# Performance work log

Measured on AMD Instinct MI355X. Metric: run time of the kernel, lower is better.

The kernel has to match this reference:

```python
import jax, jax.numpy as jnp
import numpy as np

W_IN = 128
I_DIM = 64
O_DIM = 64
B = 256
W = 64


def setup_inputs() -> dict:
    key = jax.random.key(0)
    ks = jax.random.split(key, 12)
    std = 0.01
    inp = {
        "input": jax.random.normal(ks[0], (B, W, I_DIM), jnp.float32),
        "w_embeddings": jax.random.normal(ks[1], (B, W, W_IN), jnp.float32),
        "logj": jax.random.normal(ks[2], (B, W, I_DIM), jnp.float32),
        # w_net: Linear(W_IN -> 2*W_IN), Tanh, Linear(2*W_IN -> I*O)
        "w_w1": jax.random.normal(ks[3], (2 * W_IN, W_IN), jnp.float32) * std,
        "w_b1": jnp.zeros((2 * W_IN,), jnp.float32),
        "w_w2": jax.random.normal(ks[4], (I_DIM * O_DIM, 2 * W_IN), jnp.float32) * std,
        "w_b2": jnp.zeros((I_DIM * O_DIM,), jnp.float32),
        # b_net: Linear(W_IN -> 2*W_IN), Tanh, Linear(2*W_IN -> O)
        "b_w1": jax.random.normal(ks[5], (2 * W_IN, W_IN), jnp.float32) * std,
        "b_b1": jnp.zeros((2 * W_IN,), jnp.float32),
        "b_w2": jax.random.normal(ks[6], (O_DIM, 2 * W_IN), jnp.float32) * std,
        "b_b2": jnp.zeros((O_DIM,), jnp.float32),
    }
    return inp


def reference(input, w_embeddings, logj, w_w1, w_b1, w_w2, w_b2, b_w1, b_b1, b_w2, b_b2):
    # Hypernetworks: two small MLPs over w_embeddings [B, W, W_IN]
    h_w = jnp.tanh(jnp.einsum('bwe,he->bwh', w_embeddings, w_w1) + w_b1)
    w1 = (jnp.einsum('bwh,oh->bwo', h_w, w_w2) + w_b2).reshape(B, W, I_DIM, O_DIM)

    h_b = jnp.tanh(jnp.einsum('bwe,he->bwh', w_embeddings, b_w1) + b_b1)
    b1 = jnp.einsum('bwh,oh->bwo', h_b, b_w2) + b_b2  # [B, W, O]

    # exp-weighted contraction: output[b,w,o] = sum_i input[b,w,i] * exp(w1[b,w,i,o]) + b1
    output = jnp.einsum('bwi,bwio->bwo', input, jnp.exp(w1)) + b1

    # log-Jacobian accumulation: logsumexp over input dim
    logj_out = jax.nn.logsumexp(w1 + logj[..., None], axis=-2)  # [B, W, O]
    return (output, logj_out)
```

## Files before the change

kernel.cpp:

```cpp
#include <hip/hip_runtime.h>
#include <math.h>


typedef __attribute__((ext_vector_type(8))) short s16x8;
typedef __attribute__((ext_vector_type(4))) float f32x4;

__device__ inline unsigned short f2bf(float f) {
  unsigned int u = __float_as_uint(f);
  u += 0x7fffu + ((u >> 16) & 1u);
  return (unsigned short)(u >> 16);
}
__device__ inline float bf2f(unsigned short u) { return __uint_as_float(((unsigned int)u) << 16); }
__device__ inline s16x8 cvt8(float4 a, float4 b) {
  s16x8 v;
  v[0] = (short)f2bf(a.x); v[1] = (short)f2bf(a.y); v[2] = (short)f2bf(a.z); v[3] = (short)f2bf(a.w);
  v[4] = (short)f2bf(b.x); v[5] = (short)f2bf(b.y); v[6] = (short)f2bf(b.z); v[7] = (short)f2bf(b.w);
  return v;
}
__device__ inline float fast_tanh(float x) {
  float t = __expf(2.0f * x);
  return __fdividef(t - 1.0f, t + 1.0f);
}
__device__ inline void stage16(const unsigned short* gsrc, char* ldst) {
  __builtin_amdgcn_global_load_lds(
      (const __attribute__((address_space(1))) unsigned int*)gsrc,
      (__attribute__((address_space(3))) unsigned int*)ldst, 16, 0, 0);
}

__global__ __launch_bounds__(256) void k_pre(
    const float* __restrict__ w_w2, const float* __restrict__ emb,
    const float* __restrict__ w_w1, const float* __restrict__ w_b1,
    const float* __restrict__ b_w1, const float* __restrict__ b_b1,
    const float* __restrict__ b_w2, const float* __restrict__ b_b2,
    unsigned short* __restrict__ W2F, unsigned short* __restrict__ Hw,
    float* __restrict__ b1out) {
  __shared__ __align__(16) char lsm[67584];
  const int t = threadIdx.x, l = t & 63, lo = t & 15, hi = (t >> 4) & 3, w = t >> 6;
  const int bid = blockIdx.x;

  if (bid < 64) {
    const int i = bid;
    float* ld = (float*)lsm;
    const float* src = w_w2 + (size_t)i * 16384;
    #pragma unroll
    for (int v = 0; v < 16; ++v) {
      int flat = t * 64 + v * 4;
      int row = flat >> 8, col = flat & 255;
      *(float4*)(ld + row * 264 + col) = *(const float4*)(src + flat);
    }
    __syncthreads();
    #pragma unroll
    for (int ks = 0; ks < 8; ++ks) {
      const float* p = ld + (w * 16 + lo) * 264 + ks * 32 + hi * 8;
      s16x8 vfr = cvt8(*(const float4*)p, *(const float4*)(p + 4));
      *(s16x8*)(W2F + ((size_t)(i * 4 + w) * 8 + ks) * 512 + (size_t)l * 8) = vfr;
    }
    return;
  }

  const int hb_id = bid - 64, net = hb_id & 1, mb = hb_id >> 1;
  const int mw0 = mb * 128 + w * 32;
  const float* W1 = net ? b_w1 : w_w1;
  const float* B1 = net ? b_b1 : w_b1;
  s16x8 ae[2][4];
  #pragma unroll
  for (int mt = 0; mt < 2; ++mt)
    #pragma unroll
    for (int ks = 0; ks < 4; ++ks) {
      const float* p = emb + (size_t)(mw0 + mt * 16 + lo) * 128 + ks * 32 + hi * 8;
      ae[mt][ks] = cvt8(*(const float4*)p, *(const float4*)(p + 4));
    }
  unsigned short* hb = (unsigned short*)lsm + (size_t)w * 32 * 264;
  #pragma unroll
  for (int nt = 0; nt < 16; ++nt) {
    f32x4 acc[2] = {{0,0,0,0},{0,0,0,0}};
    #pragma unroll
    for (int ks = 0; ks < 4; ++ks) {
      const float* bp = W1 + (size_t)(nt * 16 + lo) * 128 + ks * 32 + hi * 8;
      s16x8 bf = cvt8(*(const float4*)bp, *(const float4*)(bp + 4));
      acc[0] = __builtin_amdgcn_mfma_f32_16x16x32_bf16(ae[0][ks], bf, acc[0], 0, 0, 0);
      acc[1] = __builtin_amdgcn_mfma_f32_16x16x32_bf16(ae[1][ks], bf, acc[1], 0, 0, 0);
    }
    float bv = B1[nt * 16 + lo];
    #pragma unroll
    for (int mt = 0; mt < 2; ++mt)
      #pragma unroll
      for (int r = 0; r < 4; ++r) {
        float h = fast_tanh(acc[mt][r] + bv);
        if (net) hb[(mt * 16 + hi * 4 + r) * 264 + nt * 16 + lo] = f2bf(h);
        else Hw[(size_t)(mw0 + mt * 16 + hi * 4 + r) * 256 + nt * 16 + lo] = f2bf(h);
      }
  }
  if (net) {
    #pragma unroll
    for (int ot = 0; ot < 4; ++ot) {
      f32x4 acc[2] = {{0,0,0,0},{0,0,0,0}};
      #pragma unroll
      for (int ks = 0; ks < 8; ++ks) {
        const float* bp = b_w2 + (size_t)(ot * 16 + lo) * 256 + ks * 32 + hi * 8;
        s16x8 bf = cvt8(*(const float4*)bp, *(const float4*)(bp + 4));
        s16x8 a0 = *(const s16x8*)(hb + (0 * 16 + lo) * 264 + ks * 32 + hi * 8);
        s16x8 a1 = *(const s16x8*)(hb + (1 * 16 + lo) * 264 + ks * 32 + hi * 8);
        acc[0] = __builtin_amdgcn_mfma_f32_16x16x32_bf16(a0, bf, acc[0], 0, 0, 0);
        acc[1] = __builtin_amdgcn_mfma_f32_16x16x32_bf16(a1, bf, acc[1], 0, 0, 0);
      }
      float bb = b_b2[ot * 16 + lo];
      #pragma unroll
      for (int mt = 0; mt < 2; ++mt)
        #pragma unroll
        for (int r = 0; r < 4; ++r)
          b1out[(size_t)(mw0 + mt * 16 + hi * 4 + r) * 64 + ot * 16 + lo] = acc[mt][r] + bb;
    }
  }
}

__global__ __launch_bounds__(256, 2) void k_fused(
    const float* __restrict__ input, const float* __restrict__ logj,
    const float* __restrict__ w_b2,
    const unsigned short* __restrict__ W2F, const unsigned short* __restrict__ Hw,
    float* __restrict__ Poa, float* __restrict__ Pse) {
  __shared__ __align__(16) char smem[81920];
  float* xin_l = (float*)(smem + 65536);
  unsigned short* elj_l = (unsigned short*)(smem + 73728);
  unsigned short* ewb_l = (unsigned short*)(smem + 77824);

  const int t = threadIdx.x, l = t & 63, lo = t & 15, hi = (t >> 4) & 3;
  const int w = t >> 6, wu = __builtin_amdgcn_readfirstlane(w);
  const int bid = blockIdx.x;
  const int mb = bid >> 1, iq = bid & 1;
  const int m0 = mb * 64, i0 = iq * 32;

  {
    int mm = t & 63, ib = (t >> 6) * 8;
    const float* ip = input + (size_t)(m0 + mm) * 64 + i0 + ib;
    const float* lp = logj + (size_t)(m0 + mm) * 64 + i0 + ib;
    float4 v0 = *(const float4*)ip, v1 = *(const float4*)(ip + 4);
    float4 g0 = *(const float4*)lp, g1 = *(const float4*)(lp + 4);
    float vi[8] = {v0.x, v0.y, v0.z, v0.w, v1.x, v1.y, v1.z, v1.w};
    float gj[8] = {g0.x, g0.y, g0.z, g0.w, g1.x, g1.y, g1.z, g1.w};
    #pragma unroll
    for (int j = 0; j < 8; ++j) {
      xin_l[(ib + j) * 64 + mm] = vi[j];
      elj_l[(ib + j) * 64 + mm] = f2bf(__expf(gj[j]));
    }
    int il = t >> 3, ob = (t & 7) * 8;
    const float* wp = w_b2 + (size_t)(i0 + il) * 64 + ob;
    float4 e0 = *(const float4*)wp, e1 = *(const float4*)(wp + 4);
    float ev[8] = {e0.x, e0.y, e0.z, e0.w, e1.x, e1.y, e1.z, e1.w};
    #pragma unroll
    for (int j = 0; j < 8; ++j) ewb_l[il * 64 + ob + j] = f2bf(__expf(ev[j]));
  }

  s16x8 bh[4][8];
  #pragma unroll
  for (int nt = 0; nt < 4; ++nt)
    #pragma unroll
    for (int ks = 0; ks < 8; ++ks)
      bh[nt][ks] = *(const s16x8*)(Hw + (size_t)(m0 + nt * 16 + lo) * 256 + ks * 32 + hi * 8);

  __syncthreads();

  char* Ab = smem + wu * 16384;
  #pragma unroll
  for (int p = 0; p < 2; ++p)
    #pragma unroll
    for (int ks = 0; ks < 8; ++ks)
      stage16(W2F + ((size_t)(i0 + p) * 4 + wu) * 4096 + ks * 512 + (size_t)l * 8,
              Ab + p * 8192 + ks * 1024);

  f32x4 outa[4] = {{0,0,0,0},{0,0,0,0},{0,0,0,0},{0,0,0,0}};
  f32x4 sea[4] = {{0,0,0,0},{0,0,0,0},{0,0,0,0},{0,0,0,0}};

  for (int il = 0; il < 32; ++il) {
    if (il < 31) asm volatile("s_waitcnt vmcnt(8)" ::: "memory");
    else         asm volatile("s_waitcnt vmcnt(0)" ::: "memory");
    __builtin_amdgcn_sched_barrier(0);
    const char* ab = Ab + (il & 1) * 8192;

    float xin[4], el[4], ew[4];
    #pragma unroll
    for (int nt = 0; nt < 4; ++nt) {
      xin[nt] = xin_l[il * 64 + nt * 16 + lo];
      el[nt] = bf2f(elj_l[il * 64 + nt * 16 + lo]);
    }
    {
      ushort4 uv = *(const ushort4*)(ewb_l + il * 64 + wu * 16 + hi * 4);
      ew[0] = bf2f(uv.x); ew[1] = bf2f(uv.y); ew[2] = bf2f(uv.z); ew[3] = bf2f(uv.w);
    }
    f32x4 acc[4] = {{0,0,0,0},{0,0,0,0},{0,0,0,0},{0,0,0,0}};
    #pragma unroll
    for (int ks = 0; ks < 8; ++ks) {
      s16x8 a = *(const s16x8*)(ab + ks * 1024 + l * 16);
      acc[0] = __builtin_amdgcn_mfma_f32_16x16x32_bf16(a, bh[0][ks], acc[0], 0, 0, 0);
      acc[1] = __builtin_amdgcn_mfma_f32_16x16x32_bf16(a, bh[1][ks], acc[1], 0, 0, 0);
      acc[2] = __builtin_amdgcn_mfma_f32_16x16x32_bf16(a, bh[2][ks], acc[2], 0, 0, 0);
      acc[3] = __builtin_amdgcn_mfma_f32_16x16x32_bf16(a, bh[3][ks], acc[3], 0, 0, 0);
    }
    asm volatile("s_waitcnt lgkmcnt(0)" ::: "memory");
    __builtin_amdgcn_sched_barrier(0);
    if (il < 30) {
      size_t gb = ((size_t)(i0 + il + 2) * 4 + wu) * 4096;
      #pragma unroll
      for (int ks = 0; ks < 8; ++ks)
        stage16(W2F + gb + ks * 512 + (size_t)l * 8, Ab + (il & 1) * 8192 + ks * 1024);
    }
    #pragma unroll
    for (int nt = 0; nt < 4; ++nt)
      #pragma unroll
      for (int r = 0; r < 4; ++r) {
        float e1 = __expf(acc[nt][r]) * ew[r];
        outa[nt][r] = fmaf(xin[nt], e1, outa[nt][r]);
        sea[nt][r] = fmaf(el[nt], e1, sea[nt][r]);
      }
  }

  const int o0 = wu * 16 + hi * 4;
  #pragma unroll
  for (int nt = 0; nt < 4; ++nt) {
    size_t base = (size_t)(m0 + nt * 16 + lo) * 64 + o0;
    *(f32x4*)(Poa + (size_t)iq * 1048576 + base) = outa[nt];
    *(f32x4*)(Pse + (size_t)iq * 1048576 + base) = sea[nt];
  }
}

__global__ __launch_bounds__(256) void k_final(
    const float* __restrict__ b1, const float* __restrict__ Poa,
    const float* __restrict__ Pse, float* __restrict__ out) {
  int idx = (blockIdx.x * 256 + threadIdx.x) * 4;
  float4 bb = *(const float4*)(b1 + idx);
  float4 a0 = *(const float4*)(Poa + idx);
  float4 a1 = *(const float4*)(Poa + 1048576 + idx);
  float4 s0 = *(const float4*)(Pse + idx);
  float4 s1 = *(const float4*)(Pse + 1048576 + idx);
  float4 o1, o2;
  o1.x = bb.x + a0.x + a1.x; o1.y = bb.y + a0.y + a1.y;
  o1.z = bb.z + a0.z + a1.z; o1.w = bb.w + a0.w + a1.w;
  o2.x = __logf(s0.x + s1.x); o2.y = __logf(s0.y + s1.y);
  o2.z = __logf(s0.z + s1.z); o2.w = __logf(s0.w + s1.w);
  *(float4*)(out + idx) = o1;
  *(float4*)(out + 1048576 + idx) = o2;
}

extern "C" void kernel_launch(void* const* d_in, const int* in_sizes, int n_in,
                              void* d_out, int out_size, void* d_ws, size_t ws_size,
                              hipStream_t stream) {
  const float* input = (const float*)d_in[0];
  const float* w_emb = (const float*)d_in[1];
  const float* logj  = (const float*)d_in[2];
  const float* w_w1  = (const float*)d_in[3];
  const float* w_b1  = (const float*)d_in[4];
  const float* w_w2  = (const float*)d_in[5];
  const float* w_b2  = (const float*)d_in[6];
  const float* b_w1  = (const float*)d_in[7];
  const float* b_b1  = (const float*)d_in[8];
  const float* b_w2  = (const float*)d_in[9];
  const float* b_b2  = (const float*)d_in[10];
  float* out = (float*)d_out;

  char* wsb = (char*)d_ws;
  unsigned short* W2F = (unsigned short*)(wsb);
  unsigned short* Hw  = (unsigned short*)(wsb + 2097152);
  float*          b1  = (float*)(wsb + 10485760);
  float*          Poa = (float*)(wsb + 14680064);
  float*          Pse = (float*)(wsb + 23068672);

  hipLaunchKernelGGL(k_pre, dim3(320), dim3(256), 0, stream,
                     w_w2, w_emb, w_w1, w_b1, b_w1, b_b1, b_w2, b_b2, W2F, Hw, b1);
  hipLaunchKernelGGL(k_fused, dim3(512), dim3(256), 0, stream,
                     input, logj, w_b2, W2F, Hw, Poa, Pse);
  hipLaunchKernelGGL(k_final, dim3(1024), dim3(256), 0, stream, b1, Poa, Pse, out);
}
```

Before: 160.4 us.

## Split W2 staging into half-chunks, shrink pre-kernel row tiles, cache W1 in LDS

In the fused kernel, each 8-chunk W2F stage is split into two halves with separate vmcnt waits, so MFMAs on the first half can start while the second half is still loading. In the pre-kernel, each wave now handles 16 rows instead of 32 and the grid doubles to 576 blocks, raising parallelism. W1 is converted to bf16 once per block into LDS rather than reloaded from global per wave. The W2 transpose load is made coalesced, and the b_net hidden state stays in registers before a single LDS write. The cost is more waitcnt bookkeeping that must track the issue order of outstanding loads.

```diff
diff --git a/kernel.cpp b/kernel.cpp
--- a/kernel.cpp
+++ b/kernel.cpp
@@ -4,6 +4,8 @@
 
 typedef __attribute__((ext_vector_type(8))) short s16x8;
 typedef __attribute__((ext_vector_type(4))) float f32x4;
+
+#define WAITV(N) asm volatile("s_waitcnt vmcnt(" #N ")" ::: "memory")
 
 __device__ inline unsigned short f2bf(float f) {
   unsigned int u = __float_as_uint(f);
@@ -36,6 +38,7 @@
     float* __restrict__ b1out) {
   __shared__ __align__(16) char lsm[67584];
   const int t = threadIdx.x, l = t & 63, lo = t & 15, hi = (t >> 4) & 3, w = t >> 6;
+  const int wu = __builtin_amdgcn_readfirstlane(w);
   const int bid = blockIdx.x;
 
   if (bid < 64) {
@@ -44,7 +47,7 @@
     const float* src = w_w2 + (size_t)i * 16384;
     #pragma unroll
     for (int v = 0; v < 16; ++v) {
-      int flat = t * 64 + v * 4;
+      int flat = v * 1024 + t * 4;
       int row = flat >> 8, col = flat & 255;
       *(float4*)(ld + row * 264 + col) = *(const float4*)(src + flat);
     }
@@ -59,57 +62,68 @@
   }
 
   const int hb_id = bid - 64, net = hb_id & 1, mb = hb_id >> 1;
-  const int mw0 = mb * 128 + w * 32;
+  const int mw0 = mb * 64 + w * 16;
   const float* W1 = net ? b_w1 : w_w1;
   const float* B1 = net ? b_b1 : w_b1;
-  s16x8 ae[2][4];
-  #pragma unroll
-  for (int mt = 0; mt < 2; ++mt)
+
+  #pragma unroll
+  for (int j = 0; j < 16; ++j) {
+    int c = wu * 16 + j, nt = c >> 2, ks = c & 3;
+    const float* bp = W1 + (size_t)(nt * 16 + lo) * 128 + ks * 32 + hi * 8;
+    s16x8 f = cvt8(*(const float4*)bp, *(const float4*)(bp + 4));
+    *(s16x8*)(lsm + c * 1024 + l * 16) = f;
+  }
+  s16x8 ae[4];
+  #pragma unroll
+  for (int ks = 0; ks < 4; ++ks) {
+    const float* p = emb + (size_t)(mw0 + lo) * 128 + ks * 32 + hi * 8;
+    ae[ks] = cvt8(*(const float4*)p, *(const float4*)(p + 4));
+  }
+  __syncthreads();
+
+  unsigned short hreg[16][4];
+  #pragma unroll
+  for (int nt = 0; nt < 16; ++nt) {
+    f32x4 acc = {0.f, 0.f, 0.f, 0.f};
     #pragma unroll
     for (int ks = 0; ks < 4; ++ks) {
-      const float* p = emb + (size_t)(mw0 + mt * 16 + lo) * 128 + ks * 32 + hi * 8;
-      ae[mt][ks] = cvt8(*(const float4*)p, *(const float4*)(p + 4));
-    }
-  unsigned short* hb = (unsigned short*)lsm + (size_t)w * 32 * 264;
-  #pragma unroll
-  for (int nt = 0; nt < 16; ++nt) {
-    f32x4 acc[2] = {{0,0,0,0},{0,0,0,0}};
-    #pragma unroll
-    for (int ks = 0; ks < 4; ++ks) {
-      const float* bp = W1 + (size_t)(nt * 16 + lo) * 128 + ks * 32 + hi * 8;
-      s16x8 bf = cvt8(*(const float4*)bp, *(const float4*)(bp + 4));
-      acc[0] = __builtin_amdgcn_mfma_f32_16x16x32_bf16(ae[0][ks], bf, acc[0], 0, 0, 0);
-      acc[1] = __builtin_amdgcn_mfma_f32_16x16x32_bf16(ae[1][ks], bf, acc[1], 0, 0, 0);
+      s16x8 b = *(const s16x8*)(lsm + (nt * 4 + ks) * 1024 + l * 16);
+      acc = __builtin_amdgcn_mfma_f32_16x16x32_bf16(ae[ks], b, acc, 0, 0, 0);
     }
     float bv = B1[nt * 16 + lo];
     #pragma unroll
-    for (int mt = 0; mt < 2; ++mt)
-      #pragma unroll
-      for (int r = 0; r < 4; ++r) {
-        float h = fast_tanh(acc[mt][r] + bv);
-        if (net) hb[(mt * 16 + hi * 4 + r) * 264 + nt * 16 + lo] = f2bf(h);
-        else Hw[(size_t)(mw0 + mt * 16 + hi * 4 + r) * 256 + nt * 16 + lo] = f2bf(h);
-      }
+    for (int r = 0; r < 4; ++r) {
+      float h = fast_tanh(acc[r] + bv);
+      if (net) hreg[nt][r] = f2bf(h);
+      else Hw[(size_t)(mw0 + hi * 4 + r) * 256 + nt * 16 + lo] = f2bf(h);
+    }
   }
   if (net) {
+    __syncthreads();
+    unsigned short* hb = (unsigned short*)(lsm) + (size_t)wu * 4224;
+    #pragma unroll
+    for (int nt = 0; nt < 16; ++nt)
+      #pragma unroll
+      for (int r = 0; r < 4; ++r)
+        hb[(hi * 4 + r) * 264 + nt * 16 + lo] = hreg[nt][r];
+    s16x8 ab[8];
+    __builtin_amdgcn_s_waitcnt(0);
+    #pragma unroll
+    for (int ks = 0; ks < 8; ++ks)
+      ab[ks] = *(const s16x8*)(hb + lo * 264 + ks * 32 + hi * 8);
     #pragma unroll
     for (int ot = 0; ot < 4; ++ot) {
-      f32x4 acc[2] = {{0,0,0,0},{0,0,0,0}};
+      f32x4 acc2 = {0.f, 0.f, 0.f, 0.f};
       #pragma unroll
       for (int ks = 0; ks < 8; ++ks) {
         const float* bp = b_w2 + (size_t)(ot * 16 + lo) * 256 + ks * 32 + hi * 8;
         s16x8 bf = cvt8(*(const float4*)bp, *(const float4*)(bp + 4));
-        s16x8 a0 = *(const s16x8*)(hb + (0 * 16 + lo) * 264 + ks * 32 + hi * 8);
-        s16x8 a1 = *(const s16x8*)(hb + (1 * 16 + lo) * 264 + ks * 32 + hi * 8);
-        acc[0] = __builtin_amdgcn_mfma_f32_16x16x32_bf16(a0, bf, acc[0], 0, 0, 0);
-        acc[1] = __builtin_amdgcn_mfma_f32_16x16x32_bf16(a1, bf, acc[1], 0, 0, 0);
+        acc2 = __builtin_amdgcn_mfma_f32_16x16x32_bf16(ab[ks], bf, acc2, 0, 0, 0);
       }
       float bb = b_b2[ot * 16 + lo];
       #pragma unroll
-      for (int mt = 0; mt < 2; ++mt)
-        #pragma unroll
-        for (int r = 0; r < 4; ++r)
-          b1out[(size_t)(mw0 + mt * 16 + hi * 4 + r) * 64 + ot * 16 + lo] = acc[mt][r] + bb;
+      for (int r = 0; r < 4; ++r)
+        b1out[(size_t)(mw0 + hi * 4 + r) * 64 + ot * 16 + lo] = acc2[r] + bb;
     }
   }
 }
@@ -159,24 +173,19 @@
       bh[nt][ks] = *(const s16x8*)(Hw + (size_t)(m0 + nt * 16 + lo) * 256 + ks * 32 + hi * 8);
 
   __syncthreads();
+  asm volatile("s_waitcnt vmcnt(0)" ::: "memory");
+  __builtin_amdgcn_sched_barrier(0);
 
   char* Ab = smem + wu * 16384;
   #pragma unroll
-  for (int p = 0; p < 2; ++p)
-    #pragma unroll
-    for (int ks = 0; ks < 8; ++ks)
-      stage16(W2F + ((size_t)(i0 + p) * 4 + wu) * 4096 + ks * 512 + (size_t)l * 8,
-              Ab + p * 8192 + ks * 1024);
+  for (int g = 0; g < 16; ++g)
+    stage16(W2F + ((size_t)(i0 + (g >> 3)) * 4 + wu) * 4096 + (size_t)(g & 7) * 512 + (size_t)l * 8,
+            Ab + g * 1024);
 
   f32x4 outa[4] = {{0,0,0,0},{0,0,0,0},{0,0,0,0},{0,0,0,0}};
   f32x4 sea[4] = {{0,0,0,0},{0,0,0,0},{0,0,0,0},{0,0,0,0}};
 
   for (int il = 0; il < 32; ++il) {
-    if (il < 31) asm volatile("s_waitcnt vmcnt(8)" ::: "memory");
-    else         asm volatile("s_waitcnt vmcnt(0)" ::: "memory");
-    __builtin_amdgcn_sched_barrier(0);
-    const char* ab = Ab + (il & 1) * 8192;
-
     float xin[4], el[4], ew[4];
     #pragma unroll
     for (int nt = 0; nt < 4; ++nt) {
@@ -188,8 +197,12 @@
       ew[0] = bf2f(uv.x); ew[1] = bf2f(uv.y); ew[2] = bf2f(uv.z); ew[3] = bf2f(uv.w);
     }
     f32x4 acc[4] = {{0,0,0,0},{0,0,0,0},{0,0,0,0},{0,0,0,0}};
-    #pragma unroll
-    for (int ks = 0; ks < 8; ++ks) {
+    char* ab = Ab + (il & 1) * 8192;
+
+    if (il < 31) { WAITV(12); } else { WAITV(4); }
+    __builtin_amdgcn_sched_barrier(0);
+    #pragma unroll
+    for (int ks = 0; ks < 4; ++ks) {
       s16x8 a = *(const s16x8*)(ab + ks * 1024 + l * 16);
       acc[0] = __builtin_amdgcn_mfma_f32_16x16x32_bf16(a, bh[0][ks], acc[0], 0, 0, 0);
       acc[1] = __builtin_amdgcn_mfma_f32_16x16x32_bf16(a, bh[1][ks], acc[1], 0, 0, 0);
@@ -199,10 +212,28 @@
     asm volatile("s_waitcnt lgkmcnt(0)" ::: "memory");
     __builtin_amdgcn_sched_barrier(0);
     if (il < 30) {
-      size_t gb = ((size_t)(i0 + il + 2) * 4 + wu) * 4096;
-      #pragma unroll
-      for (int ks = 0; ks < 8; ++ks)
-        stage16(W2F + gb + ks * 512 + (size_t)l * 8, Ab + (il & 1) * 8192 + ks * 1024);
+      size_t gsrc = ((size_t)(i0 + il + 2) * 4 + wu) * 4096;
+      #pragma unroll
+      for (int ks = 0; ks < 4; ++ks)
+        stage16(W2F + gsrc + (size_t)ks * 512 + (size_t)l * 8, ab + ks * 1024);
+    }
+    if (il < 30) { WAITV(12); } else if (il == 30) { WAITV(8); } else { WAITV(0); }
+    __builtin_amdgcn_sched_barrier(0);
+    #pragma unroll
+    for (int ks = 4; ks < 8; ++ks) {
+      s16x8 a = *(const s16x8*)(ab + ks * 1024 + l * 16);
+      acc[0] = __builtin_amdgcn_mfma_f32_16x16x32_bf16(a, bh[0][ks], acc[0], 0, 0, 0);
+      acc[1] = __builtin_amdgcn_mfma_f32_16x16x32_bf16(a, bh[1][ks], acc[1], 0, 0, 0);
+      acc[2] = __builtin_amdgcn_mfma_f32_16x16x32_bf16(a, bh[2][ks], acc[2], 0, 0, 0);
+      acc[3] = __builtin_amdgcn_mfma_f32_16x16x32_bf16(a, bh[3][ks], acc[3], 0, 0, 0);
+    }
+    asm volatile("s_waitcnt lgkmcnt(0)" ::: "memory");
+    __builtin_amdgcn_sched_barrier(0);
+    if (il < 30) {
+      size_t gsrc = ((size_t)(i0 + il + 2) * 4 + wu) * 4096;
+      #pragma unroll
+      for (int ks = 4; ks < 8; ++ks)
+        stage16(W2F + gsrc + (size_t)ks * 512 + (size_t)l * 8, ab + ks * 1024);
     }
     #pragma unroll
     for (int nt = 0; nt < 4; ++nt)
@@ -264,7 +295,7 @@
   float*          Poa = (float*)(wsb + 14680064);
   float*          Pse = (float*)(wsb + 23068672);
 
-  hipLaunchKernelGGL(k_pre, dim3(320), dim3(256), 0, stream,
+  hipLaunchKernelGGL(k_pre, dim3(576), dim3(256), 0, stream,
                      w_w2, w_emb, w_w1, w_b1, b_w1, b_b1, b_w2, b_b2, W2F, Hw, b1);
   hipLaunchKernelGGL(k_fused, dim3(512), dim3(256), 0, stream,
                      input, logj, w_b2, W2F, Hw, Poa, Pse);
```

Measured after the change: 160.1 us. Within noise of the previous version (-0.2%).

## Fuse hypernet first layers, b-net and final reduction into main kernel

Applied to the files above, without the earlier changes.

Moves the tanh hidden-layer computation and the bias network into the main fused kernel through a swizzled LDS bounce buffer, so the Hw and b1 intermediates no longer make a round trip through global memory. The i-dimension split across two blocks is removed in favour of a 512-thread block whose two halves reduce through LDS, which eliminates the separate final kernel and the partial-sum buffers. The main GEMM switches from 16x16x32 to 32x32x16 MFMA, and the loop now overlaps the epilogue of one step with the MFMAs of the next. In exchange it runs one block per CU with 160KB of LDS, leaving little room for latency hiding, and the hidden-layer GEMM is recomputed inside the main kernel.

```diff
diff --git a/kernel.cpp b/kernel.cpp
--- a/kernel.cpp
+++ b/kernel.cpp
@@ -4,6 +4,12 @@
 
 typedef __attribute__((ext_vector_type(8))) short s16x8;
 typedef __attribute__((ext_vector_type(4))) float f32x4;
+typedef __attribute__((ext_vector_type(16))) float f32x16;
+
+#define WAITV(N) asm volatile("s_waitcnt vmcnt(" #N ")" ::: "memory")
+#define WAITLGKM0 asm volatile("s_waitcnt lgkmcnt(0)" ::: "memory")
+#define SB __builtin_amdgcn_sched_barrier(0)
+#define ZERO16 {0.f,0.f,0.f,0.f,0.f,0.f,0.f,0.f,0.f,0.f,0.f,0.f,0.f,0.f,0.f,0.f}
 
 __device__ inline unsigned short f2bf(float f) {
   unsigned int u = __float_as_uint(f);
@@ -27,113 +33,110 @@
       (__attribute__((address_space(3))) unsigned int*)ldst, 16, 0, 0);
 }
 
-__global__ __launch_bounds__(256) void k_pre(
-    const float* __restrict__ w_w2, const float* __restrict__ emb,
+__global__ __launch_bounds__(256) void k_pre(const float* __restrict__ w_w2,
+                                             unsigned short* __restrict__ W2F) {
+  __shared__ __align__(16) float ld[32 * 136];
+  const int t = threadIdx.x, l = t & 63, w = t >> 6;
+  const int b = blockIdx.x;
+  const int i = b >> 2, oq = (b >> 1) & 1, kh = b & 1;
+  const float* src = w_w2 + ((size_t)i * 64 + oq * 32) * 256 + kh * 128;
+  #pragma unroll
+  for (int v = 0; v < 4; ++v) {
+    int flat = v * 1024 + t * 4;
+    int row = flat >> 7, col = flat & 127;
+    *(float4*)(ld + row * 136 + col) = *(const float4*)(src + (size_t)row * 256 + col);
+  }
+  __syncthreads();
+  const int l31 = l & 31, l5 = l >> 5;
+  #pragma unroll
+  for (int j = 0; j < 2; ++j) {
+    int ksl = w * 2 + j;
+    const float* p = ld + l31 * 136 + ksl * 16 + l5 * 8;
+    s16x8 fr = cvt8(*(const float4*)p, *(const float4*)(p + 4));
+    *(s16x8*)(W2F + (((size_t)(i * 2 + oq) * 16) + kh * 8 + ksl) * 512 + (size_t)l * 8) = fr;
+  }
+}
+
+#define EPI_G(ACC, IABS, PART, G)                                                         \
+  { ushort4 ev = *(const ushort4*)(ewb_l + (IABS)*64 + oq*32 + (PART)*16 + (G)*8 + l5*4); \
+    float e_;                                                                             \
+    e_ = __expf(ACC[(PART)*8+(G)*4+0]) * bf2f(ev.x);                                      \
+    outa[(PART)*8+(G)*4+0] += xin_ * e_; sea[(PART)*8+(G)*4+0] += elj_ * e_;              \
+    e_ = __expf(ACC[(PART)*8+(G)*4+1]) * bf2f(ev.y);                                      \
+    outa[(PART)*8+(G)*4+1] += xin_ * e_; sea[(PART)*8+(G)*4+1] += elj_ * e_;              \
+    e_ = __expf(ACC[(PART)*8+(G)*4+2]) * bf2f(ev.z);                                      \
+    outa[(PART)*8+(G)*4+2] += xin_ * e_; sea[(PART)*8+(G)*4+2] += elj_ * e_;              \
+    e_ = __expf(ACC[(PART)*8+(G)*4+3]) * bf2f(ev.w);                                      \
+    outa[(PART)*8+(G)*4+3] += xin_ * e_; sea[(PART)*8+(G)*4+3] += elj_ * e_; }
+
+#define EPILOG(ACC, IABS, PART)                                                           \
+  { float xin_ = xin_l[(IABS)*64 + mq*32 + l31];                                          \
+    float elj_ = bf2f(elj_l[(IABS)*64 + mq*32 + l31]);                                    \
+    EPI_G(ACC, IABS, PART, 0) EPI_G(ACC, IABS, PART, 1) }
+
+#define MFMA8(ACC, H)                                                                     \
+  { s16x8 a0 = *(const s16x8*)(ring + ((H)*8+0)*1024 + l*16);                             \
+    s16x8 a1 = *(const s16x8*)(ring + ((H)*8+1)*1024 + l*16);                             \
+    s16x8 a2 = *(const s16x8*)(ring + ((H)*8+2)*1024 + l*16);                             \
+    s16x8 a3 = *(const s16x8*)(ring + ((H)*8+3)*1024 + l*16);                             \
+    s16x8 a4 = *(const s16x8*)(ring + ((H)*8+4)*1024 + l*16);                             \
+    s16x8 a5 = *(const s16x8*)(ring + ((H)*8+5)*1024 + l*16);                             \
+    s16x8 a6 = *(const s16x8*)(ring + ((H)*8+6)*1024 + l*16);                             \
+    s16x8 a7 = *(const s16x8*)(ring + ((H)*8+7)*1024 + l*16);                             \
+    __builtin_amdgcn_s_setprio(1);                                                        \
+    ACC = __builtin_amdgcn_mfma_f32_32x32x16_bf16(a0, bh[(H)*8+0], ACC, 0, 0, 0);         \
+    ACC = __builtin_amdgcn_mfma_f32_32x32x16_bf16(a1, bh[(H)*8+1], ACC, 0, 0, 0);         \
+    ACC = __builtin_amdgcn_mfma_f32_32x32x16_bf16(a2, bh[(H)*8+2], ACC, 0, 0, 0);         \
+    ACC = __builtin_amdgcn_mfma_f32_32x32x16_bf16(a3, bh[(H)*8+3], ACC, 0, 0, 0);         \
+    ACC = __builtin_amdgcn_mfma_f32_32x32x16_bf16(a4, bh[(H)*8+4], ACC, 0, 0, 0);         \
+    ACC = __builtin_amdgcn_mfma_f32_32x32x16_bf16(a5, bh[(H)*8+5], ACC, 0, 0, 0);         \
+    ACC = __builtin_amdgcn_mfma_f32_32x32x16_bf16(a6, bh[(H)*8+6], ACC, 0, 0, 0);         \
+    ACC = __builtin_amdgcn_mfma_f32_32x32x16_bf16(a7, bh[(H)*8+7], ACC, 0, 0, 0);         \
+    __builtin_amdgcn_s_setprio(0); }
+
+#define BODY_HALF(H, ACC, PRV, DOPREV, EIABS, ILAST)                                      \
+  { if (!(ILAST)) { WAITV(8); } else if ((H) == 0) { WAITV(8); } else { WAITV(0); }       \
+    SB;                                                                                   \
+    MFMA8(ACC, H)                                                                         \
+    if (DOPREV) { EPILOG(PRV, EIABS, H) }                                                 \
+    WAITLGKM0; SB;                                                                        \
+    if (!(ILAST)) {                                                                       \
+      stage16(wp + ((H)*8+0)*512, ring + ((H)*8+0)*1024);                                 \
+      stage16(wp + ((H)*8+1)*512, ring + ((H)*8+1)*1024);                                 \
+      stage16(wp + ((H)*8+2)*512, ring + ((H)*8+2)*1024);                                 \
+      stage16(wp + ((H)*8+3)*512, ring + ((H)*8+3)*1024);                                 \
+      stage16(wp + ((H)*8+4)*512, ring + ((H)*8+4)*1024);                                 \
+      stage16(wp + ((H)*8+5)*512, ring + ((H)*8+5)*1024);                                 \
+      stage16(wp + ((H)*8+6)*512, ring + ((H)*8+6)*1024);                                 \
+      stage16(wp + ((H)*8+7)*512, ring + ((H)*8+7)*1024);                                 \
+    } }
+
+__global__ __launch_bounds__(512, 1) void k_fused(
+    const float* __restrict__ input, const float* __restrict__ logj,
+    const float* __restrict__ emb,
     const float* __restrict__ w_w1, const float* __restrict__ w_b1,
     const float* __restrict__ b_w1, const float* __restrict__ b_b1,
     const float* __restrict__ b_w2, const float* __restrict__ b_b2,
-    unsigned short* __restrict__ W2F, unsigned short* __restrict__ Hw,
-    float* __restrict__ b1out) {
-  __shared__ __align__(16) char lsm[67584];
-  const int t = threadIdx.x, l = t & 63, lo = t & 15, hi = (t >> 4) & 3, w = t >> 6;
-  const int bid = blockIdx.x;
-
-  if (bid < 64) {
-    const int i = bid;
-    float* ld = (float*)lsm;
-    const float* src = w_w2 + (size_t)i * 16384;
-    #pragma unroll
-    for (int v = 0; v < 16; ++v) {
-      int flat = t * 64 + v * 4;
-      int row = flat >> 8, col = flat & 255;
-      *(float4*)(ld + row * 264 + col) = *(const float4*)(src + flat);
-    }
-    __syncthreads();
-    #pragma unroll
-    for (int ks = 0; ks < 8; ++ks) {
-      const float* p = ld + (w * 16 + lo) * 264 + ks * 32 + hi * 8;
-      s16x8 vfr = cvt8(*(const float4*)p, *(const float4*)(p + 4));
-      *(s16x8*)(W2F + ((size_t)(i * 4 + w) * 8 + ks) * 512 + (size_t)l * 8) = vfr;
-    }
-    return;
-  }
-
-  const int hb_id = bid - 64, net = hb_id & 1, mb = hb_id >> 1;
-  const int mw0 = mb * 128 + w * 32;
-  const float* W1 = net ? b_w1 : w_w1;
-  const float* B1 = net ? b_b1 : w_b1;
-  s16x8 ae[2][4];
-  #pragma unroll
-  for (int mt = 0; mt < 2; ++mt)
-    #pragma unroll
-    for (int ks = 0; ks < 4; ++ks) {
-      const float* p = emb + (size_t)(mw0 + mt * 16 + lo) * 128 + ks * 32 + hi * 8;
-      ae[mt][ks] = cvt8(*(const float4*)p, *(const float4*)(p + 4));
-    }
-  unsigned short* hb = (unsigned short*)lsm + (size_t)w * 32 * 264;
-  #pragma unroll
-  for (int nt = 0; nt < 16; ++nt) {
-    f32x4 acc[2] = {{0,0,0,0},{0,0,0,0}};
-    #pragma unroll
-    for (int ks = 0; ks < 4; ++ks) {
-      const float* bp = W1 + (size_t)(nt * 16 + lo) * 128 + ks * 32 + hi * 8;
-      s16x8 bf = cvt8(*(const float4*)bp, *(const float4*)(bp + 4));
-      acc[0] = __builtin_amdgcn_mfma_f32_16x16x32_bf16(ae[0][ks], bf, acc[0], 0, 0, 0);
-      acc[1] = __builtin_amdgcn_mfma_f32_16x16x32_bf16(ae[1][ks], bf, acc[1], 0, 0, 0);
-    }
-    float bv = B1[nt * 16 + lo];
-    #pragma unroll
-    for (int mt = 0; mt < 2; ++mt)
-      #pragma unroll
-      for (int r = 0; r < 4; ++r) {
-        float h = fast_tanh(acc[mt][r] + bv);
-        if (net) hb[(mt * 16 + hi * 4 + r) * 264 + nt * 16 + lo] = f2bf(h);
-        else Hw[(size_t)(mw0 + mt * 16 + hi * 4 + r) * 256 + nt * 16 + lo] = f2bf(h);
-      }
-  }
-  if (net) {
-    #pragma unroll
-    for (int ot = 0; ot < 4; ++ot) {
-      f32x4 acc[2] = {{0,0,0,0},{0,0,0,0}};
-      #pragma unroll
-      for (int ks = 0; ks < 8; ++ks) {
-        const float* bp = b_w2 + (size_t)(ot * 16 + lo) * 256 + ks * 32 + hi * 8;
-        s16x8 bf = cvt8(*(const float4*)bp, *(const float4*)(bp + 4));
-        s16x8 a0 = *(const s16x8*)(hb + (0 * 16 + lo) * 264 + ks * 32 + hi * 8);
-        s16x8 a1 = *(const s16x8*)(hb + (1 * 16 + lo) * 264 + ks * 32 + hi * 8);
-        acc[0] = __builtin_amdgcn_mfma_f32_16x16x32_bf16(a0, bf, acc[0], 0, 0, 0);
-        acc[1] = __builtin_amdgcn_mfma_f32_16x16x32_bf16(a1, bf, acc[1], 0, 0, 0);
-      }
-      float bb = b_b2[ot * 16 + lo];
-      #pragma unroll
-      for (int mt = 0; mt < 2; ++mt)
-        #pragma unroll
-        for (int r = 0; r < 4; ++r)
-          b1out[(size_t)(mw0 + mt * 16 + hi * 4 + r) * 64 + ot * 16 + lo] = acc[mt][r] + bb;
-    }
-  }
-}
-
-__global__ __launch_bounds__(256, 2) void k_fused(
-    const float* __restrict__ input, const float* __restrict__ logj,
     const float* __restrict__ w_b2,
-    const unsigned short* __restrict__ W2F, const unsigned short* __restrict__ Hw,
-    float* __restrict__ Poa, float* __restrict__ Pse) {
-  __shared__ __align__(16) char smem[81920];
-  float* xin_l = (float*)(smem + 65536);
-  unsigned short* elj_l = (unsigned short*)(smem + 73728);
-  unsigned short* ewb_l = (unsigned short*)(smem + 77824);
-
-  const int t = threadIdx.x, l = t & 63, lo = t & 15, hi = (t >> 4) & 3;
-  const int w = t >> 6, wu = __builtin_amdgcn_readfirstlane(w);
-  const int bid = blockIdx.x;
-  const int mb = bid >> 1, iq = bid & 1;
-  const int m0 = mb * 64, i0 = iq * 32;
+    const unsigned short* __restrict__ W2F, float* __restrict__ out) {
+  __shared__ __align__(16) char smem[163840];
+  float* xin_l = (float*)(smem + 131072);
+  unsigned short* elj_l = (unsigned short*)(smem + 147456);
+  unsigned short* ewb_l = (unsigned short*)(smem + 155648);
+
+  const int t = threadIdx.x, l = t & 63;
+  const int w = t >> 6;
+  const int wu = __builtin_amdgcn_readfirstlane(w);
+  const int tq = wu >> 2;
+  const int wq = wu & 3, oq = wq & 1, mq = wq >> 1;
+  const int lo = t & 15, hi = (t >> 4) & 3;
+  const int l31 = l & 31, l5 = l >> 5;
+  const int m0 = blockIdx.x * 64;
 
   {
     int mm = t & 63, ib = (t >> 6) * 8;
-    const float* ip = input + (size_t)(m0 + mm) * 64 + i0 + ib;
-    const float* lp = logj + (size_t)(m0 + mm) * 64 + i0 + ib;
+    const float* ip = input + (size_t)(m0 + mm) * 64 + ib;
+    const float* lp = logj + (size_t)(m0 + mm) * 64 + ib;
     float4 v0 = *(const float4*)ip, v1 = *(const float4*)(ip + 4);
     float4 g0 = *(const float4*)lp, g1 = *(const float4*)(lp + 4);
     float vi[8] = {v0.x, v0.y, v0.z, v0.w, v1.x, v1.y, v1.z, v1.w};
@@ -144,101 +147,148 @@
       elj_l[(ib + j) * 64 + mm] = f2bf(__expf(gj[j]));
     }
     int il = t >> 3, ob = (t & 7) * 8;
-    const float* wp = w_b2 + (size_t)(i0 + il) * 64 + ob;
-    float4 e0 = *(const float4*)wp, e1 = *(const float4*)(wp + 4);
+    const float* wpb = w_b2 + (size_t)il * 64 + ob;
+    float4 e0 = *(const float4*)wpb, e1 = *(const float4*)(wpb + 4);
     float ev[8] = {e0.x, e0.y, e0.z, e0.w, e1.x, e1.y, e1.z, e1.w};
     #pragma unroll
     for (int j = 0; j < 8; ++j) ewb_l[il * 64 + ob + j] = f2bf(__expf(ev[j]));
   }
 
-  s16x8 bh[4][8];
-  #pragma unroll
-  for (int nt = 0; nt < 4; ++nt)
+  const float* W1 = tq ? b_w1 : w_w1;
+  const float* B1b = tq ? b_b1 : w_b1;
+  char* bounce = smem + tq * 32768;
+  {
+    s16x8 ae[4];
+    #pragma unroll
+    for (int ks = 0; ks < 4; ++ks) {
+      const float* p = emb + (size_t)(m0 + wq * 16 + lo) * 128 + ks * 32 + hi * 8;
+      ae[ks] = cvt8(*(const float4*)p, *(const float4*)(p + 4));
+    }
+    #pragma unroll
+    for (int nt = 0; nt < 16; ++nt) {
+      f32x4 acc = {0.f, 0.f, 0.f, 0.f};
+      #pragma unroll
+      for (int ks = 0; ks < 4; ++ks) {
+        const float* bp = W1 + (size_t)(nt * 16 + lo) * 128 + ks * 32 + hi * 8;
+        s16x8 bfr = cvt8(*(const float4*)bp, *(const float4*)(bp + 4));
+        acc = __builtin_amdgcn_mfma_f32_16x16x32_bf16(ae[ks], bfr, acc, 0, 0, 0);
+      }
+      float bv = B1b[nt * 16 + lo];
+      #pragma unroll
+      for (int r = 0; r < 4; ++r) {
+        int row = wq * 16 + hi * 4 + r;
+        int byte = row * 512 + (nt * 16 + lo) * 2;
+        byte ^= ((row & 7) << 4);
+        *(unsigned short*)(bounce + byte) = f2bf(fast_tanh(acc[r] + bv));
+      }
+    }
+  }
+  __syncthreads();
+
+  s16x8 bh[16];
+  #pragma unroll
+  for (int ks = 0; ks < 16; ++ks) {
+    int row = mq * 32 + l31;
+    int byte = row * 512 + (ks * 16 + l5 * 8) * 2;
+    byte ^= ((row & 7) << 4);
+    bh[ks] = *(const s16x8*)(smem + byte);
+  }
+  f32x4 b1r[4] = {{0,0,0,0},{0,0,0,0},{0,0,0,0},{0,0,0,0}};
+  if (tq == 1) {
+    s16x8 ab[8];
+    #pragma unroll
+    for (int ks = 0; ks < 8; ++ks) {
+      int row = wq * 16 + lo;
+      int byte = row * 512 + (ks * 32 + hi * 8) * 2;
+      byte ^= ((row & 7) << 4);
+      ab[ks] = *(const s16x8*)(smem + 32768 + byte);
+    }
     #pragma unroll
     for (int ks = 0; ks < 8; ++ks)
-      bh[nt][ks] = *(const s16x8*)(Hw + (size_t)(m0 + nt * 16 + lo) * 256 + ks * 32 + hi * 8);
-
-  __syncthreads();
-
-  char* Ab = smem + wu * 16384;
-  #pragma unroll
-  for (int p = 0; p < 2; ++p)
-    #pragma unroll
-    for (int ks = 0; ks < 8; ++ks)
-      stage16(W2F + ((size_t)(i0 + p) * 4 + wu) * 4096 + ks * 512 + (size_t)l * 8,
-              Ab + p * 8192 + ks * 1024);
-
-  f32x4 outa[4] = {{0,0,0,0},{0,0,0,0},{0,0,0,0},{0,0,0,0}};
-  f32x4 sea[4] = {{0,0,0,0},{0,0,0,0},{0,0,0,0},{0,0,0,0}};
-
-  for (int il = 0; il < 32; ++il) {
-    if (il < 31) asm volatile("s_waitcnt vmcnt(8)" ::: "memory");
-    else         asm volatile("s_waitcnt vmcnt(0)" ::: "memory");
-    __builtin_amdgcn_sched_barrier(0);
-    const char* ab = Ab + (il & 1) * 8192;
-
-    float xin[4], el[4], ew[4];
-    #pragma unroll
-    for (int nt = 0; nt < 4; ++nt) {
-      xin[nt] = xin_l[il * 64 + nt * 16 + lo];
-      el[nt] = bf2f(elj_l[il * 64 + nt * 16 + lo]);
-    }
-    {
-      ushort4 uv = *(const ushort4*)(ewb_l + il * 64 + wu * 16 + hi * 4);
-      ew[0] = bf2f(uv.x); ew[1] = bf2f(uv.y); ew[2] = bf2f(uv.z); ew[3] = bf2f(uv.w);
-    }
-    f32x4 acc[4] = {{0,0,0,0},{0,0,0,0},{0,0,0,0},{0,0,0,0}};
-    #pragma unroll
-    for (int ks = 0; ks < 8; ++ks) {
-      s16x8 a = *(const s16x8*)(ab + ks * 1024 + l * 16);
-      acc[0] = __builtin_amdgcn_mfma_f32_16x16x32_bf16(a, bh[0][ks], acc[0], 0, 0, 0);
-      acc[1] = __builtin_amdgcn_mfma_f32_16x16x32_bf16(a, bh[1][ks], acc[1], 0, 0, 0);
-      acc[2] = __builtin_amdgcn_mfma_f32_16x16x32_bf16(a, bh[2][ks], acc[2], 0, 0, 0);
-      acc[3] = __builtin_amdgcn_mfma_f32_16x16x32_bf16(a, bh[3][ks], acc[3], 0, 0, 0);
-    }
-    asm volatile("s_waitcnt lgkmcnt(0)" ::: "memory");
-    __builtin_amdgcn_sched_barrier(0);
-    if (il < 30) {
-      size_t gb = ((size_t)(i0 + il + 2) * 4 + wu) * 4096;
-      #pragma unroll
-      for (int ks = 0; ks < 8; ++ks)
-        stage16(W2F + gb + ks * 512 + (size_t)l * 8, Ab + (il & 1) * 8192 + ks * 1024);
-    }
-    #pragma unroll
-    for (int nt = 0; nt < 4; ++nt)
-      #pragma unroll
-      for (int r = 0; r < 4; ++r) {
-        float e1 = __expf(acc[nt][r]) * ew[r];
-        outa[nt][r] = fmaf(xin[nt], e1, outa[nt][r]);
-        sea[nt][r] = fmaf(el[nt], e1, sea[nt][r]);
+      #pragma unroll
+      for (int ot = 0; ot < 4; ++ot) {
+        const float* bp = b_w2 + (size_t)(ot * 16 + lo) * 256 + ks * 32 + hi * 8;
+        s16x8 bfr = cvt8(*(const float4*)bp, *(const float4*)(bp + 4));
+        b1r[ot] = __builtin_amdgcn_mfma_f32_16x16x32_bf16(ab[ks], bfr, b1r[ot], 0, 0, 0);
       }
-  }
-
-  const int o0 = wu * 16 + hi * 4;
-  #pragma unroll
-  for (int nt = 0; nt < 4; ++nt) {
-    size_t base = (size_t)(m0 + nt * 16 + lo) * 64 + o0;
-    *(f32x4*)(Poa + (size_t)iq * 1048576 + base) = outa[nt];
-    *(f32x4*)(Pse + (size_t)iq * 1048576 + base) = sea[nt];
-  }
-}
-
-__global__ __launch_bounds__(256) void k_final(
-    const float* __restrict__ b1, const float* __restrict__ Poa,
-    const float* __restrict__ Pse, float* __restrict__ out) {
-  int idx = (blockIdx.x * 256 + threadIdx.x) * 4;
-  float4 bb = *(const float4*)(b1 + idx);
-  float4 a0 = *(const float4*)(Poa + idx);
-  float4 a1 = *(const float4*)(Poa + 1048576 + idx);
-  float4 s0 = *(const float4*)(Pse + idx);
-  float4 s1 = *(const float4*)(Pse + 1048576 + idx);
-  float4 o1, o2;
-  o1.x = bb.x + a0.x + a1.x; o1.y = bb.y + a0.y + a1.y;
-  o1.z = bb.z + a0.z + a1.z; o1.w = bb.w + a0.w + a1.w;
-  o2.x = __logf(s0.x + s1.x); o2.y = __logf(s0.y + s1.y);
-  o2.z = __logf(s0.z + s1.z); o2.w = __logf(s0.w + s1.w);
-  *(float4*)(out + idx) = o1;
-  *(float4*)(out + 1048576 + idx) = o2;
+    #pragma unroll
+    for (int ot = 0; ot < 4; ++ot) {
+      float bb = b_b2[ot * 16 + lo];
+      #pragma unroll
+      for (int r = 0; r < 4; ++r) b1r[ot][r] += bb;
+    }
+  }
+  __syncthreads();
+  WAITV(0); SB;
+
+  char* ring = smem + wu * 16384;
+  const int ibase = tq * 32;
+  const unsigned short* wp =
+      W2F + ((size_t)ibase * 32 + (size_t)oq * 16) * 512 + (size_t)l * 8;
+  #pragma unroll
+  for (int g = 0; g < 16; ++g) stage16(wp + g * 512, ring + g * 1024);
+  wp += 16384;
+
+  float outa[16], sea[16];
+  #pragma unroll
+  for (int z = 0; z < 16; ++z) { outa[z] = 0.f; sea[z] = 0.f; }
+  f32x16 accA, accB;
+
+  #pragma unroll 1
+  for (int u = 0; u < 16; ++u) {
+    const int e0 = ibase + 2 * u - 1, e1 = ibase + 2 * u;
+    accA = (f32x16)ZERO16;
+    BODY_HALF(0, accA, accB, (u > 0), e0, 0)
+    BODY_HALF(1, accA, accB, (u > 0), e0, 0)
+    wp += 16384;
+    accB = (f32x16)ZERO16;
+    BODY_HALF(0, accB, accA, 1, e1, (u == 15))
+    BODY_HALF(1, accB, accA, 1, e1, (u == 15))
+    if (u < 15) wp += 16384;
+  }
+  EPILOG(accB, ibase + 31, 0)
+  EPILOG(accB, ibase + 31, 1)
+
+  __syncthreads();
+  {
+    float* oaT = (float*)smem + (size_t)tq * 4224;
+    float* seT = (float*)smem + 8448 + (size_t)tq * 4224;
+    float* b1L = (float*)smem + 16896;
+    #pragma unroll
+    for (int r = 0; r < 16; ++r) {
+      int o = oq * 32 + (r & 3) + 8 * (r >> 2) + 4 * l5;
+      int m = mq * 32 + l31;
+      oaT[m * 66 + o] = outa[r];
+      seT[m * 66 + o] = sea[r];
+    }
+    if (tq == 1) {
+      #pragma unroll
+      for (int ot = 0; ot < 4; ++ot)
+        #pragma unroll
+        for (int r2 = 0; r2 < 4; ++r2)
+          b1L[(wq * 16 + hi * 4 + r2) * 66 + ot * 16 + lo] = b1r[ot][r2];
+    }
+  }
+  __syncthreads();
+  {
+    const float* base = (const float*)smem;
+    int flat = t * 8;
+    int m = flat >> 6, o = flat & 63;
+    float vo[8], vl[8];
+    #pragma unroll
+    for (int j = 0; j < 8; ++j) {
+      int idx = m * 66 + o + j;
+      vo[j] = base[idx] + base[4224 + idx] + base[16896 + idx];
+      vl[j] = __logf(base[8448 + idx] + base[8448 + 4224 + idx]);
+    }
+    size_t ob = (size_t)(m0 + m) * 64 + o;
+    float4 s0 = {vo[0], vo[1], vo[2], vo[3]}, s1 = {vo[4], vo[5], vo[6], vo[7]};
+    float4 t0 = {vl[0], vl[1], vl[2], vl[3]}, t1 = {vl[4], vl[5], vl[6], vl[7]};
+    *(float4*)(out + ob) = s0;
+    *(float4*)(out + ob + 4) = s1;
+    *(float4*)(out + 1048576 + ob) = t0;
+    *(float4*)(out + 1048576 + ob + 4) = t1;
+  }
 }
 
 extern "C" void kernel_launch(void* const* d_in, const int* in_sizes, int n_in,
@@ -257,16 +307,10 @@
   const float* b_b2  = (const float*)d_in[10];
   float* out = (float*)d_out;
 
-  char* wsb = (char*)d_ws;
-  unsigned short* W2F = (unsigned short*)(wsb);
-  unsigned short* Hw  = (unsigned short*)(wsb + 2097152);
-  float*          b1  = (float*)(wsb + 10485760);
-  float*          Poa = (float*)(wsb + 14680064);
-  float*          Pse = (float*)(wsb + 23068672);
-
-  hipLaunchKernelGGL(k_pre, dim3(320), dim3(256), 0, stream,
-                     w_w2, w_emb, w_w1, w_b1, b_w1, b_b1, b_w2, b_b2, W2F, Hw, b1);
-  hipLaunchKernelGGL(k_fused, dim3(512), dim3(256), 0, stream,
-                     input, logj, w_b2, W2F, Hw, Poa, Pse);
-  hipLaunchKernelGGL(k_final, dim3(1024), dim3(256), 0, stream, b1, Poa, Pse, out);
-}
+  unsigned short* W2F = (unsigned short*)d_ws;
+
+  hipLaunchKernelGGL(k_pre, dim3(256), dim3(256), 0, stream, w_w2, W2F);
+  hipLaunchKernelGGL(k_fused, dim3(256), dim3(512), 0, stream,
+                     input, logj, w_emb, w_w1, w_b1, b_w1, b_b1, b_w2, b_b2, w_b2,
+                     W2F, out);
+}
```

After: 175.3 us. 1.09x slower.
